# Kernel tuning notes

Hardware: AMD Instinct MI355X
Metric: run time of the kernel (lower is better)

The kernel has to match this reference:

```python
import jax, jax.numpy as jnp
import numpy as np

HEADS, BS, HALO = 8, 8, 3
WIN = BS + 2 * HALO  # 14


def setup_inputs() -> dict:
    key = jax.random.key(0)
    k1, k2, k3, k4 = jax.random.split(key, 4)
    B, C, H, W = 16, 256, 64, 64
    dim_out_qk, dim_out_v = 256, 256
    std = C ** (-0.5)
    x = jax.random.normal(k1, (B, C, H, W), jnp.float32)
    Wq = jax.random.normal(k2, (dim_out_qk, C), jnp.float32) * std
    Wkv = jax.random.normal(k3, (dim_out_qk + dim_out_v, C), jnp.float32) * std
    pos_bias = jax.random.normal(k4, (HEADS, BS * BS, WIN * WIN), jnp.float32) * 0.02
    return {"x": x, "Wq": Wq, "Wkv": Wkv, "pos_bias": pos_bias}


def reference(x, Wq, Wkv, pos_bias):
    B, C, H, W = x.shape
    dhqk = Wq.shape[0] // HEADS            # 32
    dhv = Wkv.shape[0] // HEADS - dhqk     # 32
    scale = dhqk ** (-0.5)
    nhb, nwb = H // BS, W // BS
    nb = nhb * nwb

    xl = jnp.transpose(x, (0, 2, 3, 1))    # [B, H, W, C]

    # queries: [B, heads, nb, bs^2, dhqk] (row-major within block)
    q = xl @ Wq.T
    q = q.reshape(B, nhb, BS, nwb, BS, HEADS, dhqk)
    q = q.transpose(0, 5, 1, 3, 2, 4, 6).reshape(B, HEADS, nb, BS * BS, dhqk)

    # keys/values via overlapping halo windows (zero-padded unfold)
    kv = xl @ Wkv.T                                       # [B, H, W, dim_kv]
    kv = jnp.pad(kv, ((0, 0), (HALO, HALO), (HALO, HALO), (0, 0)))
    ridx = (jnp.arange(nhb) * BS)[:, None] + jnp.arange(WIN)[None, :]
    cidx = (jnp.arange(nwb) * BS)[:, None] + jnp.arange(WIN)[None, :]
    kv = kv[:, ridx]
    kv = kv[:, :, :, cidx]
    kv = kv.transpose(0, 1, 3, 2, 4, 5).reshape(B, nb, WIN * WIN, HEADS, dhqk + dhv)
    k = kv[..., :dhqk]
    v = kv[..., dhqk:]

    attn = jnp.einsum('bhnqd,bnkhd->bhnqk', q, k) * scale + pos_bias[None, :, None]
    attn = jax.nn.softmax(attn, axis=-1)
    out = jnp.einsum('bhnqk,bnkhd->bhnqd', attn, v)       # [B, heads, nb, bs^2, dhv]

    out = out.reshape(B, HEADS, nhb, nwb, BS, BS, dhv)
    out = out.transpose(0, 1, 6, 2, 4, 3, 5).reshape(B, HEADS * dhv, H, W)
    return out
```

## Files before the change

kernel.cpp:

```cpp
#include <hip/hip_runtime.h>
#include <hip/hip_bf16.h>
#include <stdint.h>

#define HEADS 8
#define WIN 14
#define NPOS 196
#define NPAD 224
#define NB 16
#define NC 256
#define NH 64
#define NW 64
#define NP 4096
#define NKV 512
#define NOC 768

typedef __bf16 bf16_t;
typedef bf16_t bf16x8 __attribute__((ext_vector_type(8)));
typedef float f32x4 __attribute__((ext_vector_type(4)));

union Frag {
  uint4 u4;
  bf16x8 b8;
  ushort us[8];
};

__device__ __forceinline__ ushort f2bf(float f) {
  bf16_t h = (bf16_t)f;
  return __builtin_bit_cast(ushort, h);
}
__device__ __forceinline__ bf16x8 load_bf8(const float* __restrict__ p) {
  float4 a = *reinterpret_cast<const float4*>(p);
  float4 b = *reinterpret_cast<const float4*>(p + 4);
  bf16x8 r;
  r[0] = (bf16_t)a.x; r[1] = (bf16_t)a.y; r[2] = (bf16_t)a.z; r[3] = (bf16_t)a.w;
  r[4] = (bf16_t)b.x; r[5] = (bf16_t)b.y; r[6] = (bf16_t)b.z; r[7] = (bf16_t)b.w;
  return r;
}

__device__ __forceinline__ void gload_lds16(const ushort* g, ushort* l) {
#if __has_builtin(__builtin_amdgcn_global_load_lds)
  __builtin_amdgcn_global_load_lds(
      (const __attribute__((address_space(1))) unsigned int*)(const void*)g,
      (__attribute__((address_space(3))) unsigned int*)(void*)l, 16, 0, 0);
#else
  *reinterpret_cast<uint4*>(l) = *reinterpret_cast<const uint4*>(g);
#endif
}

__device__ ushort g_wb[NOC * NC];
__device__ float g_pbt[HEADS * NPAD * 64];

__global__ __launch_bounds__(256) void k_wcast(const float* __restrict__ wq,
                                               const float* __restrict__ wkv) {
  int idx = (blockIdx.x * 256 + threadIdx.x) * 8;
  int oc = idx >> 8, c = idx & 255;
  const float* src = (oc < 256) ? (wq + (size_t)oc * NC + c)
                                : (wkv + (size_t)(oc - 256) * NC + c);
  Frag v;
  v.b8 = load_bf8(src);
  *reinterpret_cast<uint4*>(g_wb + idx) = v.u4;
}

__global__ __launch_bounds__(256) void k_pbt(const float* __restrict__ pb) {
  const int h = blockIdx.y;
  const int key = blockIdx.x * 4 + (threadIdx.x >> 6);
  const int q = threadIdx.x & 63;
  float v = -30000.0f;
  if (key < NPOS) v = pb[((size_t)(h * 64 + q)) * NPOS + key];
  g_pbt[((size_t)(h * NPAD) + key) * 64 + q] = v;
}

__global__ __launch_bounds__(256) void k_xt(const float* __restrict__ x,
                                            ushort* __restrict__ xt) {
  __shared__ __align__(16) ushort ls[64][66];
  const int b = blockIdx.z, p0 = blockIdx.x * 64, c0 = blockIdx.y * 64;
  const int by8 = blockIdx.y * 8;
  const int tid = threadIdx.x;
  #pragma unroll
  for (int it = 0; it < 4; ++it) {
    int i = it * 256 + tid;
    int c = i >> 4, ps = (i & 15) * 4;
    float4 v = *reinterpret_cast<const float4*>(x + ((size_t)(b * NC + c0 + c)) * NP + p0 + ps);
    ls[ps + 0][c] = f2bf(v.x);
    ls[ps + 1][c] = f2bf(v.y);
    ls[ps + 2][c] = f2bf(v.z);
    ls[ps + 3][c] = f2bf(v.w);
  }
  __syncthreads();
  #pragma unroll
  for (int it = 0; it < 2; ++it) {
    int i = it * 256 + tid;
    int p = i >> 3, gl = i & 7;
    Frag o;
    #pragma unroll
    for (int j = 0; j < 8; ++j) o.us[j] = ls[p][gl * 8 + j];
    int gph = by8 + (gl ^ (p & 7));
    *reinterpret_cast<uint4*>(xt + ((size_t)(b * NP) + p0 + p) * NC + gph * 8) = o.u4;
  }
}

__global__ __launch_bounds__(256, 2) void k_proj2(const ushort* __restrict__ xt,
                                                  ushort* __restrict__ qkv) {
  __shared__ __align__(16) ushort As[128 * 256];
  const int row0 = blockIdx.x * 128;
  const int n0 = blockIdx.y * 256;
  const int tid = threadIdx.x, lane = tid & 63, wid = tid >> 6;
  const int quad = lane >> 4, lc = lane & 15;
  const ushort* gs = xt + (size_t)row0 * NC;
  #pragma unroll
  for (int it = 0; it < 16; ++it) {
    int f = it * 256 + tid;
    gload_lds16(gs + (size_t)f * 8, As + f * 8);
  }
  __syncthreads();
  const int wm = (wid & 1) * 64, wn = (wid >> 1) * 128;
  f32x4 acc[4][8] = {};
  #pragma unroll
  for (int ks = 0; ks < 8; ++ks) {
    const int k0 = ks * 32 + quad * 8;
    Frag a[4];
    #pragma unroll
    for (int mt = 0; mt < 4; ++mt) {
      int row = wm + mt * 16 + lc;
      int gk = (ks * 4 + quad) ^ (lc & 7);
      a[mt].u4 = *reinterpret_cast<const uint4*>(&As[row * 256 + gk * 8]);
    }
    #pragma unroll
    for (int ng = 0; ng < 2; ++ng) {
      Frag bb[4];
      #pragma unroll
      for (int j = 0; j < 4; ++j) {
        int oc = n0 + wn + (ng * 4 + j) * 16 + lc;
        bb[j].u4 = *reinterpret_cast<const uint4*>(g_wb + (size_t)oc * NC + k0);
      }
      #pragma unroll
      for (int mt = 0; mt < 4; ++mt)
        #pragma unroll
        for (int j = 0; j < 4; ++j)
          acc[mt][ng * 4 + j] = __builtin_amdgcn_mfma_f32_16x16x32_bf16(
              a[mt].b8, bb[j].b8, acc[mt][ng * 4 + j], 0, 0, 0);
    }
  }
  __syncthreads();
  #pragma unroll
  for (int mt = 0; mt < 4; ++mt)
    #pragma unroll
    for (int nn = 0; nn < 8; ++nn) {
      int row = wm + mt * 16 + quad * 4;
      #pragma unroll
      for (int r = 0; r < 4; ++r) {
        int rr = row + r;
        int col = wn + nn * 16 + lc;
        As[rr * 256 + (((col >> 3) ^ (rr & 7)) * 8) + (col & 7)] = f2bf(acc[mt][nn][r]);
      }
    }
  __syncthreads();
  #pragma unroll
  for (int it = 0; it < 16; ++it) {
    int i = it * 256 + tid;
    int r = i >> 5, g = i & 31;
    uint4 u = *reinterpret_cast<const uint4*>(&As[r * 256 + ((g ^ (r & 7)) * 8)]);
    *reinterpret_cast<uint4*>(qkv + ((size_t)(row0 + r)) * NOC + n0 + g * 8) = u;
  }
}

__global__ __launch_bounds__(256) void k_attn_f2(const ushort* __restrict__ qkv,
                                                 float* __restrict__ out) {
  __shared__ __align__(16) ushort ksh[NPAD][40];
  __shared__ __align__(16) ushort vth[32][232];
  __shared__ __align__(16) ushort psh[4][16][32];
  float (*osh)[33] = reinterpret_cast<float(*)[33]>(&ksh[0][0]);
  const int b = blockIdx.z, h = blockIdx.y, blk = blockIdx.x;
  const int by = blk >> 3, bx = blk & 7;
  const int tid = threadIdx.x, lane = tid & 63, w = tid >> 6;
  const int quad = lane >> 4, lc = lane & 15;

  Frag aq;
  {
    int q = w * 16 + lc;
    int py = by * 8 + (q >> 3), px = bx * 8 + (q & 7);
    aq.u4 = *reinterpret_cast<const uint4*>(
        qkv + ((size_t)(b * NP + py * NW + px)) * NOC + h * 32 + quad * 8);
  }

  for (int it = 0; it < 7; ++it) {
    int i = it * 256 + tid;
    int pos = i >> 3, seg = i & 7;
    Frag v;
    v.u4 = make_uint4(0u, 0u, 0u, 0u);
    if (pos < NPOS) {
      int wy = pos / WIN;
      int wx = pos - wy * WIN;
      int yq = by * 8 - 3 + wy, xx = bx * 8 - 3 + wx;
      if ((unsigned)yq < (unsigned)NH && (unsigned)xx < (unsigned)NW)
        v.u4 = *reinterpret_cast<const uint4*>(
            qkv + ((size_t)(b * NP + yq * NW + xx)) * NOC + 256 + h * 64 + seg * 8);
    }
    if (seg < 4) {
      *reinterpret_cast<uint4*>(&ksh[pos][seg * 8]) = v.u4;
    } else {
      int d0 = (seg - 4) * 8;
      int cp = pos ^ ((seg - 4) << 3);
      #pragma unroll
      for (int j = 0; j < 8; ++j) vth[d0 + j][cp] = v.us[j];
    }
  }
  __syncthreads();

  f32x4 s[14];
  #pragma unroll
  for (int nt = 0; nt < 14; ++nt) {
    Frag bk;
    bk.u4 = *reinterpret_cast<const uint4*>(&ksh[nt * 16 + lc][quad * 8]);
    f32x4 z = {0.f, 0.f, 0.f, 0.f};
    s[nt] = __builtin_amdgcn_mfma_f32_16x16x32_bf16(aq.b8, bk.b8, z, 0, 0, 0);
  }

  const float scale = 0.17677669529663687f;
  const int qi = w * 16 + quad * 4;
  const float* __restrict__ pbh = g_pbt + (size_t)h * (NPAD * 64);
  float lsum[4] = {0.f, 0.f, 0.f, 0.f};
  #pragma unroll
  for (int nt = 0; nt < 14; ++nt) {
    int col = nt * 16 + lc;
    float4 bv = *reinterpret_cast<const float4*>(pbh + col * 64 + qi);
    #pragma unroll
    for (int r = 0; r < 4; ++r) {
      float p = __expf(s[nt][r] * scale + (&bv.x)[r]);
      s[nt][r] = p;
      lsum[r] += p;
    }
  }

  f32x4 o[2] = {};
  #pragma unroll
  for (int kt = 0; kt < 7; ++kt) {
    #pragma unroll
    for (int t = 0; t < 2; ++t)
      #pragma unroll
      for (int r = 0; r < 4; ++r)
        psh[w][quad * 4 + r][t * 16 + lc] = f2bf(s[2 * kt + t][r]);
    Frag ap;
    ap.u4 = *reinterpret_cast<const uint4*>(&psh[w][lc][quad * 8]);
    #pragma unroll
    for (int t = 0; t < 2; ++t) {
      int d = t * 16 + lc;
      int g = (kt * 4 + quad) ^ ((d >> 3) & 3);
      Frag bv;
      bv.u4 = *reinterpret_cast<const uint4*>(&vth[d][g * 8]);
      o[t] = __builtin_amdgcn_mfma_f32_16x16x32_bf16(ap.b8, bv.b8, o[t], 0, 0, 0);
    }
  }

  #pragma unroll
  for (int m = 1; m < 16; m <<= 1)
    #pragma unroll
    for (int r = 0; r < 4; ++r) lsum[r] += __shfl_xor(lsum[r], m);
  float rinv[4];
  #pragma unroll
  for (int r = 0; r < 4; ++r) rinv[r] = 1.0f / lsum[r];

  __syncthreads();
  #pragma unroll
  for (int t = 0; t < 2; ++t)
    #pragma unroll
    for (int r = 0; r < 4; ++r)
      osh[w * 16 + quad * 4 + r][t * 16 + lc] = o[t][r] * rinv[r];
  __syncthreads();

  {
    int d = tid >> 3, yy = tid & 7;
    float4 o0, o1;
    o0.x = osh[yy * 8 + 0][d]; o0.y = osh[yy * 8 + 1][d];
    o0.z = osh[yy * 8 + 2][d]; o0.w = osh[yy * 8 + 3][d];
    o1.x = osh[yy * 8 + 4][d]; o1.y = osh[yy * 8 + 5][d];
    o1.z = osh[yy * 8 + 6][d]; o1.w = osh[yy * 8 + 7][d];
    float* op = out + ((size_t)(b * NC + h * 32 + d) * NH + by * 8 + yy) * NW + bx * 8;
    *reinterpret_cast<float4*>(op) = o0;
    *reinterpret_cast<float4*>(op + 4) = o1;
  }
}

__global__ __launch_bounds__(256) void k_proj_r4(const float* __restrict__ x,
                                                 const float* __restrict__ wq,
                                                 const float* __restrict__ wkv,
                                                 ushort* __restrict__ qkv) {
  __shared__ __align__(16) ushort As[64][264];
  const int b = blockIdx.z, y = blockIdx.x;
  const int n0 = blockIdx.y * 256;
  const int tid = threadIdx.x, lane = tid & 63, wid = tid >> 6;
  const int quad = lane >> 4, lc = lane & 15;
  #pragma unroll
  for (int it = 0; it < 16; ++it) {
    int i = it * 256 + tid;
    int c = i >> 4, xs = (i & 15) * 4;
    float4 v = *reinterpret_cast<const float4*>(x + ((size_t)(b * NC + c)) * NP + y * NW + xs);
    #pragma unroll
    for (int j = 0; j < 4; ++j) {
      int row = xs + j;
      float f = (j == 0) ? v.x : (j == 1) ? v.y : (j == 2) ? v.z : v.w;
      As[row][c ^ ((((row >> 2) & 3)) << 3)] = f2bf(f);
    }
  }
  __syncthreads();
  const int wm = (wid & 1) * 32, wn = (wid >> 1) * 128;
  const int swz = ((lc >> 2) & 3) << 3;
  f32x4 acc[2][8] = {};
  #pragma unroll
  for (int ks = 0; ks < 8; ++ks) {
    const int k0 = ks * 32 + quad * 8;
    Frag a0, a1;
    a0.u4 = *reinterpret_cast<const uint4*>(&As[wm + lc][k0 ^ swz]);
    a1.u4 = *reinterpret_cast<const uint4*>(&As[wm + 16 + lc][k0 ^ swz]);
    #pragma unroll
    for (int nh = 0; nh < 2; ++nh) {
      bf16x8 bb[4];
      #pragma unroll
      for (int nt = 0; nt < 4; ++nt) {
        int oc = n0 + wn + nh * 64 + nt * 16 + lc;
        const float* wp = (oc < 256) ? (wq + (size_t)oc * NC) : (wkv + (size_t)(oc - 256) * NC);
        bb[nt] = load_bf8(wp + k0);
      }
      #pragma unroll
      for (int nt = 0; nt < 4; ++nt) {
        acc[0][nh * 4 + nt] = __builtin_amdgcn_mfma_f32_16x16x32_bf16(a0.b8, bb[nt], acc[0][nh * 4 + nt], 0, 0, 0);
        acc[1][nh * 4 + nt] = __builtin_amdgcn_mfma_f32_16x16x32_bf16(a1.b8, bb[nt], acc[1][nh * 4 + nt], 0, 0, 0);
      }
    }
  }
  __syncthreads();
  #pragma unroll
  for (int mt = 0; mt < 2; ++mt)
    #pragma unroll
    for (int nn = 0; nn < 8; ++nn)
      #pragma unroll
      for (int r = 0; r < 4; ++r)
        As[wm + mt * 16 + quad * 4 + r][wn + nn * 16 + lc] = f2bf(acc[mt][nn][r]);
  __syncthreads();
  #pragma unroll
  for (int v8 = 0; v8 < 8; ++v8) {
    int flat = v8 * 256 + tid;
    int p = flat >> 5, seg = flat & 31;
    uint4 u = *reinterpret_cast<const uint4*>(&As[p][seg * 8]);
    *reinterpret_cast<uint4*>(qkv + ((size_t)(b * NP) + y * NW + p) * NOC + n0 + seg * 8) = u;
  }
}

__global__ __launch_bounds__(256) void k_kv(const float* __restrict__ x,
                                            const float* __restrict__ wkv,
                                            ushort* __restrict__ kvb) {
  __shared__ __align__(16) ushort As[64][264];
  const int b = blockIdx.z;
  const int y = blockIdx.x;
  const int n0 = blockIdx.y * 128;
  const int tid = threadIdx.x;
  const int lane = tid & 63, wid = tid >> 6;
  const int quad = lane >> 4, lc = lane & 15;
  #pragma unroll
  for (int it = 0; it < 16; ++it) {
    int i = it * 256 + tid;
    int c = i >> 4, xs = (i & 15) * 4;
    float4 v = *reinterpret_cast<const float4*>(x + ((size_t)(b * NC + c)) * NP + y * NW + xs);
    As[xs + 0][c] = f2bf(v.x);
    As[xs + 1][c] = f2bf(v.y);
    As[xs + 2][c] = f2bf(v.z);
    As[xs + 3][c] = f2bf(v.w);
  }
  __syncthreads();
  const int wm = (wid & 1) * 32, wn = (wid >> 1) * 64;
  f32x4 acc[2][4] = {};
  #pragma unroll
  for (int ks = 0; ks < 8; ++ks) {
    const int k0 = ks * 32 + quad * 8;
    Frag a[2];
    bf16x8 bb[4];
    #pragma unroll
    for (int mt = 0; mt < 2; ++mt)
      a[mt].u4 = *reinterpret_cast<const uint4*>(&As[wm + mt * 16 + lc][k0]);
    #pragma unroll
    for (int nt = 0; nt < 4; ++nt) {
      int oc = n0 + wn + nt * 16 + lc;
      bb[nt] = load_bf8(wkv + (size_t)oc * NC + k0);
    }
    #pragma unroll
    for (int mt = 0; mt < 2; ++mt)
      #pragma unroll
      for (int nt = 0; nt < 4; ++nt)
        acc[mt][nt] = __builtin_amdgcn_mfma_f32_16x16x32_bf16(a[mt].b8, bb[nt], acc[mt][nt], 0, 0, 0);
  }
  #pragma unroll
  for (int mt = 0; mt < 2; ++mt) {
    #pragma unroll
    for (int r = 0; r < 4; ++r) {
      int pl = wm + mt * 16 + quad * 4 + r;
      #pragma unroll
      for (int nt = 0; nt < 4; ++nt) {
        int oc = n0 + wn + nt * 16 + lc;
        kvb[((size_t)(b * NP + y * NW + pl)) * NKV + oc] = f2bf(acc[mt][nt][r]);
      }
    }
  }
}

__global__ __launch_bounds__(256) void k_attn_v3(const float* __restrict__ x,
                                                 const float* __restrict__ wq,
                                                 const ushort* __restrict__ kvb,
                                                 const float* __restrict__ pbias,
                                                 float* __restrict__ out) {
  __shared__ __align__(16) ushort ksh[NPAD][40];
  __shared__ __align__(16) ushort vth[32][232];
  __shared__ __align__(16) ushort psh[4][16][232];
  __shared__ __align__(16) ushort qsh[4][16][32];
  __shared__ __align__(16) float osh[64][33];
  const int b = blockIdx.z, h = blockIdx.y, blk = blockIdx.x;
  const int by = blk >> 3, bx = blk & 7;
  const int tid = threadIdx.x, lane = tid & 63, w = tid >> 6;
  const int quad = lane >> 4, lc = lane & 15;

  for (int it = 0; it < 7; ++it) {
    int i = it * 256 + tid;
    int pos = i >> 3, seg = i & 7;
    Frag v;
    v.u4 = make_uint4(0u, 0u, 0u, 0u);
    if (pos < NPOS) {
      int wy = pos / WIN;
      int wx = pos - wy * WIN;
      int yq = by * 8 - 3 + wy, xx = bx * 8 - 3 + wx;
      if ((unsigned)yq < (unsigned)NH && (unsigned)xx < (unsigned)NW)
        v.u4 = *reinterpret_cast<const uint4*>(
            kvb + ((size_t)(b * NP + yq * NW + xx)) * NKV + h * 64 + seg * 8);
    }
    if (seg < 4) {
      *reinterpret_cast<uint4*>(&ksh[pos][seg * 8]) = v.u4;
    } else {
      int d0 = (seg - 4) * 8;
      #pragma unroll
      for (int j = 0; j < 8; ++j) vth[d0 + j][pos] = v.us[j];
    }
  }

  f32x4 qacc[2] = {};
  {
    const int q = w * 16 + lc;
    const size_t p = (size_t)(by * 8 + (q >> 3)) * NW + bx * 8 + (q & 7);
    #pragma unroll
    for (int ks = 0; ks < 8; ++ks) {
      const int k0 = ks * 32 + quad * 8;
      Frag ax;
      #pragma unroll
      for (int j = 0; j < 8; ++j)
        ax.us[j] = f2bf(x[((size_t)(b * NC + k0 + j)) * NP + p]);
      bf16x8 bw0 = load_bf8(wq + (size_t)(h * 32 + lc) * NC + k0);
      bf16x8 bw1 = load_bf8(wq + (size_t)(h * 32 + 16 + lc) * NC + k0);
      qacc[0] = __builtin_amdgcn_mfma_f32_16x16x32_bf16(ax.b8, bw0, qacc[0], 0, 0, 0);
      qacc[1] = __builtin_amdgcn_mfma_f32_16x16x32_bf16(ax.b8, bw1, qacc[1], 0, 0, 0);
    }
  }
  #pragma unroll
  for (int t = 0; t < 2; ++t)
    #pragma unroll
    for (int r = 0; r < 4; ++r)
      qsh[w][quad * 4 + r][t * 16 + lc] = f2bf(qacc[t][r]);
  Frag aq;
  aq.u4 = *reinterpret_cast<const uint4*>(&qsh[w][lc][quad * 8]);

  __syncthreads();

  f32x4 s[14];
  #pragma unroll
  for (int nt = 0; nt < 14; ++nt) {
    Frag bk;
    bk.u4 = *reinterpret_cast<const uint4*>(&ksh[nt * 16 + lc][quad * 8]);
    f32x4 z = {0.f, 0.f, 0.f, 0.f};
    s[nt] = __builtin_amdgcn_mfma_f32_16x16x32_bf16(aq.b8, bk.b8, z, 0, 0, 0);
  }

  const float scale = 0.17677669529663687f;
  const int qi = w * 16 + quad * 4;
  float lsum[4] = {0.f, 0.f, 0.f, 0.f};
  #pragma unroll
  for (int nt = 0; nt < 14; ++nt) {
    int col = nt * 16 + lc;
    #pragma unroll
    for (int r = 0; r < 4; ++r) {
      float p = 0.f;
      if (col < NPOS)
        p = __expf(s[nt][r] * scale + pbias[(size_t)(h * 64 + qi + r) * NPOS + col]);
      s[nt][r] = p;
      lsum[r] += p;
    }
  }
  #pragma unroll
  for (int m = 1; m < 16; m <<= 1) {
    #pragma unroll
    for (int r = 0; r < 4; ++r) lsum[r] += __shfl_xor(lsum[r], m);
  }
  #pragma unroll
  for (int nt = 0; nt < 14; ++nt) {
    #pragma unroll
    for (int r = 0; r < 4; ++r) psh[w][quad * 4 + r][nt * 16 + lc] = f2bf(s[nt][r]);
  }
  f32x4 o[2] = {};
  #pragma unroll
  for (int kt = 0; kt < 7; ++kt) {
    Frag ap;
    ap.u4 = *reinterpret_cast<const uint4*>(&psh[w][lc][kt * 32 + quad * 8]);
    #pragma unroll
    for (int t = 0; t < 2; ++t) {
      Frag bv;
      bv.u4 = *reinterpret_cast<const uint4*>(&vth[t * 16 + lc][kt * 32 + quad * 8]);
      o[t] = __builtin_amdgcn_mfma_f32_16x16x32_bf16(ap.b8, bv.b8, o[t], 0, 0, 0);
    }
  }
  #pragma unroll
  for (int t = 0; t < 2; ++t)
    #pragma unroll
    for (int r = 0; r < 4; ++r)
      osh[w * 16 + quad * 4 + r][t * 16 + lc] = o[t][r] / lsum[r];
  __syncthreads();
  {
    int d = tid >> 3, yy = tid & 7;
    float4 o0, o1;
    o0.x = osh[yy * 8 + 0][d]; o0.y = osh[yy * 8 + 1][d];
    o0.z = osh[yy * 8 + 2][d]; o0.w = osh[yy * 8 + 3][d];
    o1.x = osh[yy * 8 + 4][d]; o1.y = osh[yy * 8 + 5][d];
    o1.z = osh[yy * 8 + 6][d]; o1.w = osh[yy * 8 + 7][d];
    float* op = out + ((size_t)(b * NC + h * 32 + d) * NH + by * 8 + yy) * NW + bx * 8;
    *reinterpret_cast<float4*>(op) = o0;
    *reinterpret_cast<float4*>(op + 4) = o1;
  }
}

extern "C" void kernel_launch(void* const* d_in, const int* in_sizes, int n_in,
                              void* d_out, int out_size, void* d_ws, size_t ws_size,
                              hipStream_t stream) {
  const float* x   = (const float*)d_in[0];
  const float* wq  = (const float*)d_in[1];
  const float* wkv = (const float*)d_in[2];
  const float* pb  = (const float*)d_in[3];
  float* outp = (float*)d_out;

  const size_t qkv_bytes = (size_t)NB * NP * NOC * sizeof(ushort);
  const size_t xt_bytes  = (size_t)NB * NP * NC * sizeof(ushort);

  if (ws_size >= qkv_bytes + xt_bytes) {
    ushort* qkv = (ushort*)d_ws;
    ushort* xt  = (ushort*)((char*)d_ws + qkv_bytes);
    k_wcast<<<dim3(NOC * NC / (256 * 8)), 256, 0, stream>>>(wq, wkv);
    k_pbt<<<dim3(NPAD / 4, HEADS), 256, 0, stream>>>(pb);
    k_xt<<<dim3(NP / 64, NC / 64, NB), 256, 0, stream>>>(x, xt);
    k_proj2<<<dim3(NB * NP / 128, 3), 256, 0, stream>>>(xt, qkv);
    k_attn_f2<<<dim3(64, HEADS, NB), 256, 0, stream>>>(qkv, outp);
  } else if (ws_size >= qkv_bytes) {
    ushort* qkv = (ushort*)d_ws;
    k_pbt<<<dim3(NPAD / 4, HEADS), 256, 0, stream>>>(pb);
    k_proj_r4<<<dim3(NH, 3, NB), 256, 0, stream>>>(x, wq, wkv, qkv);
    k_attn_f2<<<dim3(64, HEADS, NB), 256, 0, stream>>>(qkv, outp);
  } else {
    ushort* kvb = (ushort*)d_ws;
    k_kv<<<dim3(NH, NKV / 128, NB), 256, 0, stream>>>(x, wkv, kvb);
    k_attn_v3<<<dim3(64, HEADS, NB), 256, 0, stream>>>(x, wq, kvb, pb, outp);
  }
}
```

Measured before the change: 303.2 us.

## Merge prep kernels, remap attention grid for XCD locality, use exp2 and setprio

After: 297.7 us. About the same (-1.8%).

```diff
diff --git a/kernel.cpp b/kernel.cpp
--- a/kernel.cpp
+++ b/kernel.cpp
@@ -48,26 +48,29 @@
 }
 
 __device__ ushort g_wb[NOC * NC];
-__device__ float g_pbt[HEADS * NPAD * 64];
-
-__global__ __launch_bounds__(256) void k_wcast(const float* __restrict__ wq,
-                                               const float* __restrict__ wkv) {
-  int idx = (blockIdx.x * 256 + threadIdx.x) * 8;
-  int oc = idx >> 8, c = idx & 255;
-  const float* src = (oc < 256) ? (wq + (size_t)oc * NC + c)
-                                : (wkv + (size_t)(oc - 256) * NC + c);
-  Frag v;
-  v.b8 = load_bf8(src);
-  *reinterpret_cast<uint4*>(g_wb + idx) = v.u4;
-}
-
-__global__ __launch_bounds__(256) void k_pbt(const float* __restrict__ pb) {
-  const int h = blockIdx.y;
-  const int key = blockIdx.x * 4 + (threadIdx.x >> 6);
-  const int q = threadIdx.x & 63;
-  float v = -30000.0f;
-  if (key < NPOS) v = pb[((size_t)(h * 64 + q)) * NPOS + key];
-  g_pbt[((size_t)(h * NPAD) + key) * 64 + q] = v;
+__device__ float g_pbt[HEADS * 64 * NPAD];
+
+__global__ __launch_bounds__(256) void k_prep(const float* __restrict__ wq,
+                                              const float* __restrict__ wkv,
+                                              const float* __restrict__ pb) {
+  const int wg = blockIdx.x;
+  if (wg < 96) {
+    int idx = (wg * 256 + threadIdx.x) * 8;
+    int oc = idx >> 8, c = idx & 255;
+    const float* src = (oc < 256) ? (wq + (size_t)oc * NC + c)
+                                  : (wkv + (size_t)(oc - 256) * NC + c);
+    Frag v;
+    v.b8 = load_bf8(src);
+    *reinterpret_cast<uint4*>(g_wb + idx) = v.u4;
+  } else {
+    int row = wg - 96;
+    int key = threadIdx.x;
+    if (key < NPAD) {
+      float v = -100000.0f;
+      if (key < NPOS) v = pb[(size_t)row * NPOS + key] * 1.4426950408889634f;
+      g_pbt[(size_t)row * NPAD + key] = v;
+    }
+  }
 }
 
 __global__ __launch_bounds__(256) void k_xt(const float* __restrict__ x,
@@ -170,7 +173,11 @@
   __shared__ __align__(16) ushort vth[32][232];
   __shared__ __align__(16) ushort psh[4][16][32];
   float (*osh)[33] = reinterpret_cast<float(*)[33]>(&ksh[0][0]);
-  const int b = blockIdx.z, h = blockIdx.y, blk = blockIdx.x;
+  const int orig = blockIdx.x;
+  const int wgid = (orig & 7) * 1024 + (orig >> 3);
+  const int h = wgid & 7;
+  const int blk = (wgid >> 3) & 63;
+  const int b = wgid >> 9;
   const int by = blk >> 3, bx = blk & 7;
   const int tid = threadIdx.x, lane = tid & 63, w = tid >> 6;
   const int quad = lane >> 4, lc = lane & 15;
@@ -183,6 +190,7 @@
         qkv + ((size_t)(b * NP + py * NW + px)) * NOC + h * 32 + quad * 8);
   }
 
+  #pragma unroll
   for (int it = 0; it < 7; ++it) {
     int i = it * 256 + tid;
     int pos = i >> 3, seg = i & 7;
@@ -208,6 +216,7 @@
   __syncthreads();
 
   f32x4 s[14];
+  __builtin_amdgcn_s_setprio(1);
   #pragma unroll
   for (int nt = 0; nt < 14; ++nt) {
     Frag bk;
@@ -215,18 +224,18 @@
     f32x4 z = {0.f, 0.f, 0.f, 0.f};
     s[nt] = __builtin_amdgcn_mfma_f32_16x16x32_bf16(aq.b8, bk.b8, z, 0, 0, 0);
   }
-
-  const float scale = 0.17677669529663687f;
+  __builtin_amdgcn_s_setprio(0);
+
+  const float ck = 0.17677669529663687f * 1.4426950408889634f;
   const int qi = w * 16 + quad * 4;
-  const float* __restrict__ pbh = g_pbt + (size_t)h * (NPAD * 64);
+  const float* __restrict__ pbh = g_pbt + (size_t)(h * 64) * NPAD;
   float lsum[4] = {0.f, 0.f, 0.f, 0.f};
   #pragma unroll
   for (int nt = 0; nt < 14; ++nt) {
     int col = nt * 16 + lc;
-    float4 bv = *reinterpret_cast<const float4*>(pbh + col * 64 + qi);
     #pragma unroll
     for (int r = 0; r < 4; ++r) {
-      float p = __expf(s[nt][r] * scale + (&bv.x)[r]);
+      float p = exp2f(s[nt][r] * ck + pbh[(size_t)(qi + r) * NPAD + col]);
       s[nt][r] = p;
       lsum[r] += p;
     }
@@ -242,6 +251,7 @@
         psh[w][quad * 4 + r][t * 16 + lc] = f2bf(s[2 * kt + t][r]);
     Frag ap;
     ap.u4 = *reinterpret_cast<const uint4*>(&psh[w][lc][quad * 8]);
+    __builtin_amdgcn_s_setprio(1);
     #pragma unroll
     for (int t = 0; t < 2; ++t) {
       int d = t * 16 + lc;
@@ -250,6 +260,7 @@
       bv.u4 = *reinterpret_cast<const uint4*>(&vth[d][g * 8]);
       o[t] = __builtin_amdgcn_mfma_f32_16x16x32_bf16(ap.b8, bv.b8, o[t], 0, 0, 0);
     }
+    __builtin_amdgcn_s_setprio(0);
   }
 
   #pragma unroll
@@ -546,16 +557,15 @@
   if (ws_size >= qkv_bytes + xt_bytes) {
     ushort* qkv = (ushort*)d_ws;
     ushort* xt  = (ushort*)((char*)d_ws + qkv_bytes);
-    k_wcast<<<dim3(NOC * NC / (256 * 8)), 256, 0, stream>>>(wq, wkv);
-    k_pbt<<<dim3(NPAD / 4, HEADS), 256, 0, stream>>>(pb);
+    k_prep<<<dim3(608), 256, 0, stream>>>(wq, wkv, pb);
     k_xt<<<dim3(NP / 64, NC / 64, NB), 256, 0, stream>>>(x, xt);
     k_proj2<<<dim3(NB * NP / 128, 3), 256, 0, stream>>>(xt, qkv);
-    k_attn_f2<<<dim3(64, HEADS, NB), 256, 0, stream>>>(qkv, outp);
+    k_attn_f2<<<dim3(NB * HEADS * 64), 256, 0, stream>>>(qkv, outp);
   } else if (ws_size >= qkv_bytes) {
     ushort* qkv = (ushort*)d_ws;
-    k_pbt<<<dim3(NPAD / 4, HEADS), 256, 0, stream>>>(pb);
+    k_prep<<<dim3(608), 256, 0, stream>>>(wq, wkv, pb);
     k_proj_r4<<<dim3(NH, 3, NB), 256, 0, stream>>>(x, wq, wkv, qkv);
-    k_attn_f2<<<dim3(64, HEADS, NB), 256, 0, stream>>>(qkv, outp);
+    k_attn_f2<<<dim3(NB * HEADS * 64), 256, 0, stream>>>(qkv, outp);
   } else {
     ushort* kvb = (ushort*)d_ws;
     k_kv<<<dim3(NH, NKV / 128, NB), 256, 0, stream>>>(x, wkv, kvb);
```
